# Optimization experiments

Measured on AMD Instinct MI355X. Metric: run time of the kernel, lower is better.

## Reference

```python
import jax, jax.numpy as jnp
import numpy as np
from jax import lax

PROP_TIME = 18
K_F = 3
NUM = K_F * K_F - 1   # 8 non-center taps
IDX_REF = NUM // 2    # 4


def _bilinear(img, ys, xs):
    """img: (H,W). ys/xs: (T,H,W) absolute coords. Zero padding outside."""
    H, W = img.shape
    y0 = jnp.floor(ys)
    x0 = jnp.floor(xs)
    wy = ys - y0
    wx = xs - x0
    y0i = y0.astype(jnp.int32)
    x0i = x0.astype(jnp.int32)

    def g(yi, xi):
        valid = (yi >= 0) & (yi < H) & (xi >= 0) & (xi < W)
        v = img[jnp.clip(yi, 0, H - 1), jnp.clip(xi, 0, W - 1)]
        return jnp.where(valid, v, 0.0)

    v00 = g(y0i, x0i)
    v01 = g(y0i, x0i + 1)
    v10 = g(y0i + 1, x0i)
    v11 = g(y0i + 1, x0i + 1)
    return (v00 * (1 - wy) * (1 - wx) + v01 * (1 - wy) * wx
            + v10 * wy * (1 - wx) + v11 * wy * wx)


_sample_b = jax.vmap(_bilinear, in_axes=(0, 0, 0))  # batched over B


def setup_inputs() -> dict:
    key = jax.random.key(0)
    k1, k2, k3, k4, k5 = jax.random.split(key, 5)
    B, H, W = 4, 480, 640
    CH_G = 8
    return {
        "feat_init": jax.random.uniform(k1, (B, 1, H, W), dtype=jnp.float32),
        "guidance": jax.random.normal(k2, (B, CH_G, H, W), dtype=jnp.float32),
        "confidence": jax.random.uniform(k3, (B, 1, H, W), dtype=jnp.float32),
        "w_oa": jax.random.normal(k4, (3 * NUM, CH_G, 3, 3), dtype=jnp.float32) * 0.1,
        "b_oa": jax.random.normal(k5, (3 * NUM,), dtype=jnp.float32) * 0.01,
        "aff_scale_const": jnp.ones((1,), jnp.float32) * (0.5 * NUM),  # gamma*num (TGASS)
    }


def reference(feat_init, guidance, confidence, w_oa, b_oa, aff_scale_const):
    B, _, H, W = guidance.shape

    # offset / affinity head: Conv2d(ch_g, 3*num, k=3, pad=1)
    oa = lax.conv_general_dilated(
        guidance, w_oa, window_strides=(1, 1), padding=((1, 1), (1, 1)),
        dimension_numbers=("NCHW", "OIHW", "NCHW")) + b_oa[None, :, None, None]
    o1, o2, aff = jnp.split(oa, 3, axis=1)  # each (B, 8, H, W): dy, dx, raw aff

    # insert zero offset for the center (reference) tap -> 9 taps
    z = jnp.zeros((B, 1, H, W), o1.dtype)
    off_y = jnp.concatenate([o1[:, :IDX_REF], z, o1[:, IDX_REF:]], axis=1)  # (B,9,H,W)
    off_x = jnp.concatenate([o2[:, :IDX_REF], z, o2[:, IDX_REF:]], axis=1)

    # TGASS affinity
    aff = jnp.tanh(aff) / (aff_scale_const + 1e-8)

    # confidence propagation: 1x1 deform conv per non-center tap with w_conf=1,
    # modulation=1 -> bilinear sample of confidence at p + offset (offset detached)
    nc = jnp.array([0, 1, 2, 3, 5, 6, 7, 8])
    base_y = jnp.arange(H, dtype=jnp.float32)[:, None]
    base_x = jnp.arange(W, dtype=jnp.float32)[None, :]
    yc = base_y[None, None] + lax.stop_gradient(off_y[:, nc])  # (B,8,H,W)
    xc = base_x[None, None] + lax.stop_gradient(off_x[:, nc])
    conf_aff = _sample_b(confidence[:, 0], yc, xc)             # (B,8,H,W)
    aff = aff * conf_aff

    # absolute-sum normalization (TGASS: clamp denom at 1)
    s = jnp.sum(jnp.abs(aff), axis=1, keepdims=True) + 1e-4
    s = jnp.maximum(s, 1.0)
    aff = aff / s
    aff_ref = 1.0 - jnp.sum(aff, axis=1, keepdims=True)
    aff9 = jnp.concatenate([aff[:, :IDX_REF], aff_ref, aff[:, IDX_REF:]], axis=1)
    aff9 = jax.nn.softmax(aff9, axis=1)  # (B,9,H,W)

    # propagation sampling coords: p + kernel_tap + learned offset (fixed per iter)
    kh = jnp.repeat(jnp.arange(-1, 2, dtype=jnp.float32), 3)  # (9,)
    kw = jnp.tile(jnp.arange(-1, 2, dtype=jnp.float32), 3)
    ys = base_y[None, None] + kh[None, :, None, None] + off_y  # (B,9,H,W)
    xs = base_x[None, None] + kw[None, :, None, None] + off_x

    def step(feat, _):
        samp = _sample_b(feat[:, 0], ys, xs)                  # (B,9,H,W)
        new = jnp.sum(aff9 * samp, axis=1, keepdims=True)     # (B,1,H,W)
        return new, None

    feat_result, _ = lax.scan(step, feat_init, None, length=PROP_TIME)
    return feat_result
```

## Files before the change

### kernel.cpp

```cpp
#include <hip/hip_runtime.h>
#include <hip/hip_fp16.h>
#include <math.h>

#define BB 4
#define HH 480
#define WW 640
#define HW (HH * WW)
#define PP (BB * HW)

__device__ __forceinline__ float ldz(const float* __restrict__ img, int y, int x) {
    bool v = ((unsigned)y < (unsigned)HH) & ((unsigned)x < (unsigned)WW);
    int off = v ? (y * WW + x) : 0;
    float val = img[off];
    return v ? val : 0.0f;
}

__device__ __forceinline__ void axis_map(int y0, float wy, int H,
                                         int& c0, float& t, float& s) {
    if (y0 >= 0 && y0 <= H - 2)      { c0 = y0;    t = wy;   s = 1.0f; }
    else if (y0 == -1)               { c0 = 0;     t = 0.0f; s = wy; }
    else if (y0 == H - 1)            { c0 = H - 2; t = 1.0f; s = 1.0f - wy; }
    else                             { c0 = 0;     t = 0.0f; s = 0.0f; }
}

__global__ void transpose_w_kernel(const float* __restrict__ w_oa, float* __restrict__ wT) {
    for (int i = threadIdx.x; i < 1728; i += 256) {
        const int k = i / 192;
        const int r = i - k * 192;
        const int ci = r / 24;
        const int c = r - ci * 24;
        wT[i] = w_oa[c * 72 + ci * 9 + k];
    }
}

__global__ __launch_bounds__(256) void precompute_kernel(
    const float* __restrict__ guidance,
    const float* __restrict__ confidence,
    const float* __restrict__ wT,
    const float* __restrict__ b_oa,
    const float* __restrict__ aff_scale,
    float* __restrict__ AFF,
    uint2* __restrict__ BT,
    float* __restrict__ affC)
{
    const int p = blockIdx.x * 256 + threadIdx.x;
    const int b = p / HW;
    const int rem = p - b * HW;
    const int y = rem / WW;
    const int x = rem - y * WW;

    float acc[24];
    #pragma unroll
    for (int c = 0; c < 24; ++c) acc[c] = b_oa[c];

    const float* gb = guidance + (size_t)b * 8 * HW;

    #pragma unroll 1
    for (int kidx = 0; kidx < 9; ++kidx) {
        const int yy = y + kidx / 3 - 1;
        const int xx = x + kidx % 3 - 1;
        const bool valid = ((unsigned)yy < (unsigned)HH) & ((unsigned)xx < (unsigned)WW);
        const int base = valid ? (yy * WW + xx) : 0;
        float g[8];
        #pragma unroll
        for (int ci = 0; ci < 8; ++ci) {
            float v = gb[ci * HW + base];
            g[ci] = valid ? v : 0.0f;
        }
        const float* wk = wT + kidx * 192;
        #pragma unroll
        for (int ci = 0; ci < 8; ++ci) {
            const float gv = g[ci];
            #pragma unroll
            for (int c = 0; c < 24; ++c)
                acc[c] = fmaf(gv, wk[ci * 24 + c], acc[c]);
        }
    }

    const float inv_scale = 1.0f / (aff_scale[0] + 1e-8f);
    const float* cb = confidence + (size_t)b * HW;
    const float fy = (float)y, fx = (float)x;

    float affv[8];
    #pragma unroll
    for (int j = 0; j < 8; ++j) {
        const float oy = acc[j], ox = acc[8 + j];
        const float a = tanhf(acc[16 + j]) * inv_scale;
        const float ysj = fy + oy, xsj = fx + ox;
        const float y0f = floorf(ysj), x0f = floorf(xsj);
        const float wy = ysj - y0f, wx = xsj - x0f;
        const int y0 = (int)y0f, x0 = (int)x0f;
        const float v00 = ldz(cb, y0, x0),     v01 = ldz(cb, y0, x0 + 1);
        const float v10 = ldz(cb, y0 + 1, x0), v11 = ldz(cb, y0 + 1, x0 + 1);
        const float conf = v00 * (1.0f - wy) * (1.0f - wx) + v01 * (1.0f - wy) * wx
                         + v10 * wy * (1.0f - wx)          + v11 * wy * wx;
        affv[j] = a * conf;
    }

    float s = 1e-4f;
    #pragma unroll
    for (int j = 0; j < 8; ++j) s += fabsf(affv[j]);
    s = fmaxf(s, 1.0f);
    const float inv_s = 1.0f / s;
    float sum = 0.0f;
    #pragma unroll
    for (int j = 0; j < 8; ++j) { affv[j] *= inv_s; sum += affv[j]; }
    const float aref = 1.0f - sum;

    float m = aref;
    #pragma unroll
    for (int j = 0; j < 8; ++j) m = fmaxf(m, affv[j]);
    float e[8];
    float denom = 0.0f;
    #pragma unroll
    for (int j = 0; j < 8; ++j) { e[j] = expf(affv[j] - m); denom += e[j]; }
    denom += expf(aref - m);
    const float invden = 1.0f / denom;

    affC[p] = expf(aref - m) * invden;

    #pragma unroll
    for (int j = 0; j < 8; ++j) {
        const int t9 = (j < 4) ? j : j + 1;
        const float khv = (float)(t9 / 3 - 1);
        const float kwv = (float)(t9 % 3 - 1);
        const float ys = (fy + khv) + acc[j];
        const float xs = (fx + kwv) + acc[8 + j];
        const float y0f = floorf(ys), x0f = floorf(xs);
        const float wy = ys - y0f, wx = xs - x0f;
        int y0c, x0c; float ty, tx, sy, sx;
        axis_map((int)y0f, wy, HH, y0c, ty, sy);
        axis_map((int)x0f, wx, WW, x0c, tx, sx);

        AFF[j * PP + p] = (e[j] * invden) * sy * sx;
        __half2 h2 = __floats2half2_rn(ty, tx);
        BT[(size_t)j * PP + p] = make_uint2((unsigned)(y0c * WW + x0c),
                                            __builtin_bit_cast(unsigned, h2));
    }
}

__global__ __launch_bounds__(256) void prop_kernel(
    const float* __restrict__ src,
    float* __restrict__ dst,
    const float* __restrict__ AFF,
    const uint2* __restrict__ BT,
    const float* __restrict__ affC)
{
    const int p = blockIdx.x * 256 + threadIdx.x;
    const int b = p / HW;
    const float* fb = src + (size_t)b * HW;

    float acc = affC[p] * src[p];

    #pragma unroll
    for (int j = 0; j < 8; ++j) {
        const float a = AFF[j * PP + p];
        const uint2 bt = BT[(size_t)j * PP + p];
        const float* g = fb + bt.x;
        const float v00 = g[0], v01 = g[1];
        const float v10 = g[WW], v11 = g[WW + 1];
        const __half2 h2 = __builtin_bit_cast(__half2, bt.y);
        const float2 t = __half22float2(h2);
        const float top = fmaf(t.y, v01 - v00, v00);
        const float bot = fmaf(t.y, v11 - v10, v10);
        acc = fmaf(a, fmaf(t.x, bot - top, top), acc);
    }
    dst[p] = acc;
}

extern "C" void kernel_launch(void* const* d_in, const int* in_sizes, int n_in,
                              void* d_out, int out_size, void* d_ws, size_t ws_size,
                              hipStream_t stream) {
    const float* feat_init  = (const float*)d_in[0];
    const float* guidance   = (const float*)d_in[1];
    const float* confidence = (const float*)d_in[2];
    const float* w_oa       = (const float*)d_in[3];
    const float* b_oa       = (const float*)d_in[4];
    const float* aff_scale  = (const float*)d_in[5];
    float* out = (float*)d_out;
    float* ws  = (float*)d_ws;

    const size_t need = (size_t)26 * PP * sizeof(float);
    if (ws_size < need) return;

    float* AFF  = ws;
    uint2* BT   = reinterpret_cast<uint2*>(ws + (size_t)8 * PP);
    float* affC = ws + (size_t)24 * PP;
    float* bufA = ws + (size_t)25 * PP;
    float* wT   = bufA;

    const int grid = PP / 256;
    transpose_w_kernel<<<1, 256, 0, stream>>>(w_oa, wT);
    precompute_kernel<<<grid, 256, 0, stream>>>(guidance, confidence, wT, b_oa,
                                                aff_scale, AFF, BT, affC);

    const float* src = feat_init;
    for (int i = 0; i < 18; ++i) {
        float* dst = (i & 1) ? out : bufA;
        prop_kernel<<<grid, 256, 0, stream>>>(src, dst, AFF, BT, affC);
        src = dst;
    }
}
```

Before: 598.2 us.

## Pack quantized affinity with tap index and interleave per-pixel tap data

Each tap's affinity is quantized to 13-bit fixed point and packed with the 19-bit base index into one word. All eight taps' words and half-precision bilinear weights are stored interleaved per pixel as four uint4 records, read with vector loads. This cuts the per-iteration streamed bytes in the 18 propagation passes and replaces scalar corner loads with float2 loads. In exchange, the affinities lose precision, and the error can accumulate across iterations. The float2 loads may also be unaligned when the index is odd.

```diff
diff --git a/kernel.cpp b/kernel.cpp
--- a/kernel.cpp
+++ b/kernel.cpp
@@ -39,8 +39,7 @@
     const float* __restrict__ wT,
     const float* __restrict__ b_oa,
     const float* __restrict__ aff_scale,
-    float* __restrict__ AFF,
-    uint2* __restrict__ BT,
+    uint4* __restrict__ PK4,
     float* __restrict__ affC)
 {
     const int p = blockIdx.x * 256 + threadIdx.x;
@@ -117,8 +116,9 @@
     denom += expf(aref - m);
     const float invden = 1.0f / denom;
 
-    affC[p] = expf(aref - m) * invden;
-
+    affC[p] = expf(aref - m) * invden * 8192.0f;
+
+    unsigned ba[8], tt[8];
     #pragma unroll
     for (int j = 0; j < 8; ++j) {
         const int t9 = (j < 4) ? j : j + 1;
@@ -132,40 +132,52 @@
         axis_map((int)y0f, wy, HH, y0c, ty, sy);
         axis_map((int)x0f, wx, WW, x0c, tx, sx);
 
-        AFF[j * PP + p] = (e[j] * invden) * sy * sx;
+        const float aeff = (e[j] * invden) * sy * sx;
+        unsigned aq = __float2uint_rn(aeff * 8192.0f);
+        aq = aq > 8191u ? 8191u : aq;
+        ba[j] = ((unsigned)(y0c * WW + x0c) << 13) | aq;
         __half2 h2 = __floats2half2_rn(ty, tx);
-        BT[(size_t)j * PP + p] = make_uint2((unsigned)(y0c * WW + x0c),
-                                            __builtin_bit_cast(unsigned, h2));
-    }
+        tt[j] = __builtin_bit_cast(unsigned, h2);
+    }
+    PK4[4 * p + 0] = make_uint4(ba[0], tt[0], ba[1], tt[1]);
+    PK4[4 * p + 1] = make_uint4(ba[2], tt[2], ba[3], tt[3]);
+    PK4[4 * p + 2] = make_uint4(ba[4], tt[4], ba[5], tt[5]);
+    PK4[4 * p + 3] = make_uint4(ba[6], tt[6], ba[7], tt[7]);
 }
 
 __global__ __launch_bounds__(256) void prop_kernel(
     const float* __restrict__ src,
     float* __restrict__ dst,
-    const float* __restrict__ AFF,
-    const uint2* __restrict__ BT,
+    const uint4* __restrict__ PK4,
     const float* __restrict__ affC)
 {
     const int p = blockIdx.x * 256 + threadIdx.x;
     const int b = p / HW;
     const float* fb = src + (size_t)b * HW;
 
-    float acc = affC[p] * src[p];
-
-    #pragma unroll
-    for (int j = 0; j < 8; ++j) {
-        const float a = AFF[j * PP + p];
-        const uint2 bt = BT[(size_t)j * PP + p];
-        const float* g = fb + bt.x;
-        const float v00 = g[0], v01 = g[1];
-        const float v10 = g[WW], v11 = g[WW + 1];
-        const __half2 h2 = __builtin_bit_cast(__half2, bt.y);
-        const float2 t = __half22float2(h2);
-        const float top = fmaf(t.y, v01 - v00, v00);
-        const float bot = fmaf(t.y, v11 - v10, v10);
-        acc = fmaf(a, fmaf(t.x, bot - top, top), acc);
-    }
-    dst[p] = acc;
+    const uint4 q0 = PK4[4 * p + 0];
+    const uint4 q1 = PK4[4 * p + 1];
+    const uint4 q2 = PK4[4 * p + 2];
+    const uint4 q3 = PK4[4 * p + 3];
+
+    float acc = 0.0f;
+
+    auto tap = [&](unsigned bav, unsigned tw) {
+        const float af = (float)(bav & 8191u);
+        const float* g = fb + (bav >> 13);
+        const float2 top2 = *reinterpret_cast<const float2*>(g);
+        const float2 bot2 = *reinterpret_cast<const float2*>(g + WW);
+        const float2 t = __half22float2(__builtin_bit_cast(__half2, tw));
+        const float top = fmaf(t.y, top2.y - top2.x, top2.x);
+        const float bot = fmaf(t.y, bot2.y - bot2.x, bot2.x);
+        acc = fmaf(af, fmaf(t.x, bot - top, top), acc);
+    };
+    tap(q0.x, q0.y); tap(q0.z, q0.w);
+    tap(q1.x, q1.y); tap(q1.z, q1.w);
+    tap(q2.x, q2.y); tap(q2.z, q2.w);
+    tap(q3.x, q3.y); tap(q3.z, q3.w);
+
+    dst[p] = fmaf(affC[p], src[p], acc) * (1.0f / 8192.0f);
 }
 
 extern "C" void kernel_launch(void* const* d_in, const int* in_sizes, int n_in,
@@ -180,24 +192,23 @@
     float* out = (float*)d_out;
     float* ws  = (float*)d_ws;
 
-    const size_t need = (size_t)26 * PP * sizeof(float);
+    const size_t need = (size_t)18 * PP * sizeof(float);
     if (ws_size < need) return;
 
-    float* AFF  = ws;
-    uint2* BT   = reinterpret_cast<uint2*>(ws + (size_t)8 * PP);
-    float* affC = ws + (size_t)24 * PP;
-    float* bufA = ws + (size_t)25 * PP;
+    uint4* PK4  = reinterpret_cast<uint4*>(ws);
+    float* affC = ws + (size_t)16 * PP;
+    float* bufA = ws + (size_t)17 * PP;
     float* wT   = bufA;
 
     const int grid = PP / 256;
     transpose_w_kernel<<<1, 256, 0, stream>>>(w_oa, wT);
     precompute_kernel<<<grid, 256, 0, stream>>>(guidance, confidence, wT, b_oa,
-                                                aff_scale, AFF, BT, affC);
+                                                aff_scale, PK4, affC);
 
     const float* src = feat_init;
     for (int i = 0; i < 18; ++i) {
         float* dst = (i & 1) ? out : bufA;
-        prop_kernel<<<grid, 256, 0, stream>>>(src, dst, AFF, BT, affC);
+        prop_kernel<<<grid, 256, 0, stream>>>(src, dst, PK4, affC);
         src = dst;
     }
 }
```

After: 562.5 us. 6.0% less time.
